# Optimization experiments

Measured on AMD Instinct MI355X. Metric: run time of the kernel, lower is better.

Reference implementation:

```python
import jax, jax.numpy as jnp
import numpy as np


def setup_inputs() -> dict:
    key = jax.random.key(0)
    kk, kq, kv = jax.random.split(key, 3)
    B, N, S, D = 2, 16, 2048, 64
    return {
        "k": jax.random.normal(kk, (B, N, S, D), dtype=jnp.float32),
        "q": jax.random.normal(kq, (B, N, S, D), dtype=jnp.float32),
        "v": jax.random.normal(kv, (B, N, S, D), dtype=jnp.float32),
    }


def reference(k, q, v):
    # NOTE: module applies no 1/sqrt(d) scaling (inputs pre-scaled upstream).
    attn_scores = jnp.einsum("bnqd,bnkd->bnqk", q, k)  # [B, N, Sq, Sk]
    attn_probs = jax.nn.softmax(attn_scores, axis=-1)
    # dropout p=0.0 -> identity
    attn_output = jnp.einsum("bnqk,bnkd->bnqd", attn_probs, v)
    return (attn_output, attn_probs)
```

## Files before the change

### kernel.cpp

```cpp
#include <hip/hip_runtime.h>

typedef _Float16 f16;
typedef _Float16 f16x8 __attribute__((ext_vector_type(8)));
typedef float f32x4 __attribute__((ext_vector_type(4)));

#define HEADS 32
#define SEQ   2048
#define DIM   64
#define QT    64
#define KT    64
#define NT    32
#define L2E   1.44269504088896340736f

__device__ __forceinline__ void gload_lds16(const void* gsrc, void* ldst) {
  __builtin_amdgcn_global_load_lds((__attribute__((address_space(1))) void*)gsrc,
                                   (__attribute__((address_space(3))) void*)ldst, 16, 0, 0);
}

__global__ __launch_bounds__(256) void prep_kernel(const float* __restrict__ k,
                                                   const float* __restrict__ v,
                                                   char* __restrict__ kt,
                                                   f16* __restrict__ vt) {
  int n = blockIdx.x * 256 + threadIdx.x;
  const int HALF = HEADS * SEQ * (DIM / 8);
  if (n < HALF) {
    int d8 = (n & 7) * 8;
    int kv = (n >> 3) & (SEQ - 1);
    int h  = n >> 14;
    const float* src = k + ((size_t)(h * SEQ + kv)) * DIM + d8;
    float4 a = *(const float4*)src;
    float4 b = *(const float4*)(src + 4);
    f16x8 o;
    o[0]=(f16)a.x; o[1]=(f16)a.y; o[2]=(f16)a.z; o[3]=(f16)a.w;
    o[4]=(f16)b.x; o[5]=(f16)b.y; o[6]=(f16)b.z; o[7]=(f16)b.w;
    *(f16x8*)(kt + ((size_t)(h * SEQ + kv)) * 128 + ((d8 * 2) ^ ((kv & 7) << 4))) = o;
  } else {
    int m = n - HALF;
    int d   = m & 63;
    int kv8 = ((m >> 6) & 255) * 8;
    int h   = m >> 14;
    const float* src = v + ((size_t)(h * SEQ + kv8)) * DIM + d;
    f16x8 o;
#pragma unroll
    for (int i = 0; i < 8; i++) o[i] = (f16)src[i * DIM];
    *(f16x8*)(vt + ((size_t)(h * DIM + d)) * SEQ + kv8) = o;
  }
}

#define STAGE(t, buf)                                                                  \
  do {                                                                                 \
    const char* ktile_ = kthead + (size_t)(t) * KT * 128;                              \
    gload_lds16(ktile_ + tid * 16, &lds_k[buf][tid * 16]);                             \
    gload_lds16(ktile_ + 4096 + tid * 16, &lds_k[buf][4096 + tid * 16]);               \
  } while (0)

#define QKT_M(SC, buf)                                                                 \
  do {                                                                                 \
    _Pragma("unroll") for (int kc = 0; kc < 2; kc++) {                                 \
      _Pragma("unroll") for (int f = 0; f < 4; f++) {                                  \
        int row_ = f * 16 + c;                                                         \
        f16x8 kb_ = *(const f16x8*)&lds_k[buf][row_ * 128 +                            \
                       ((kc * 64 + g * 16) ^ ((row_ & 7) << 4))];                      \
        SC[f] = __builtin_amdgcn_mfma_f32_16x16x32_f16(qa[kc], kb_, SC[f], 0, 0, 0);   \
      }                                                                                \
    }                                                                                  \
  } while (0)

#define LOAD_QA                                                                        \
  do {                                                                                 \
    const float* qp = q + ((size_t)(head * SEQ + q0 + w * 16 + c)) * DIM + g * 8;      \
    _Pragma("unroll") for (int kc = 0; kc < 2; kc++) {                                 \
      float4 a = *(const float4*)(qp + kc * 32);                                       \
      float4 b = *(const float4*)(qp + kc * 32 + 4);                                   \
      qa[kc][0]=(f16)a.x; qa[kc][1]=(f16)a.y; qa[kc][2]=(f16)a.z; qa[kc][3]=(f16)a.w;  \
      qa[kc][4]=(f16)b.x; qa[kc][5]=(f16)b.y; qa[kc][6]=(f16)b.z; qa[kc][7]=(f16)b.w;  \
    }                                                                                  \
  } while (0)

__global__ __launch_bounds__(256, 4) void lsum_kernel(const float* __restrict__ q,
                                                      const char* __restrict__ kt,
                                                      float* __restrict__ lsum) {
  __shared__ char lds_k[2][KT * 128];

  const int tid = threadIdx.x;
  const int w = tid >> 6, l = tid & 63, g = l >> 4, c = l & 15;
  const int swz  = (blockIdx.x & 7) * 128 + (blockIdx.x >> 3);
  const int head = swz >> 5;
  const int q0   = (swz & 31) * QT;

  f16x8 qa[2];
  LOAD_QA;
  const char* kthead = kt + (size_t)head * SEQ * 128;

  float l_ln[4] = {0.f, 0.f, 0.f, 0.f};
  STAGE(0, 0);
  __syncthreads();
  for (int t = 0; t < NT; t++) {
    int cur = t & 1;
    if (t + 1 < NT) STAGE(t + 1, cur ^ 1);
    f32x4 sc[4];
#pragma unroll
    for (int f = 0; f < 4; f++) sc[f] = (f32x4){0.f, 0.f, 0.f, 0.f};
    QKT_M(sc, cur);
#pragma unroll
    for (int f = 0; f < 4; f++)
#pragma unroll
      for (int r = 0; r < 4; r++) l_ln[r] += __builtin_amdgcn_exp2f(sc[f][r] * L2E);
    __syncthreads();
  }
#pragma unroll
  for (int r = 0; r < 4; r++) {
    float lv = l_ln[r];
#pragma unroll
    for (int d = 1; d < 16; d <<= 1) lv += __shfl_xor(lv, d, 64);
    if (c == 0) lsum[head * SEQ + q0 + w * 16 + 4 * g + r] = lv;
  }
}

__global__ __launch_bounds__(256, 4) void attn_kernel(const float* __restrict__ q,
                                                      const char* __restrict__ kt,
                                                      const f16* __restrict__ vt,
                                                      const float* __restrict__ lsum,
                                                      float* __restrict__ out_o,
                                                      float* __restrict__ out_p) {
  __shared__ char  lds_k[2][KT * 128];
  __shared__ float lds_pt[QT * 64];

  const int tid = threadIdx.x;
  const int w = tid >> 6, l = tid & 63, g = l >> 4, c = l & 15;
  const int swz  = (blockIdx.x & 7) * 128 + (blockIdx.x >> 3);
  const int head = swz >> 5;
  const int q0   = (swz & 31) * QT;

  f16x8 qa[2];
  LOAD_QA;

  const char* kthead = kt + (size_t)head * SEQ * 128;
  const f16*  vhead  = vt + (size_t)head * DIM * SEQ;

  f32x4 rinv;
#pragma unroll
  for (int r = 0; r < 4; r++)
    rinv[r] = 1.0f / lsum[head * SEQ + q0 + w * 16 + 4 * g + r];

  f32x4 o_acc[4];
#pragma unroll
  for (int f = 0; f < 4; f++) o_acc[f] = (f32x4){0.f, 0.f, 0.f, 0.f};
  float* prow = out_p + (size_t)(head * SEQ + q0) * SEQ;

  STAGE(0, 0);
  __syncthreads();
  for (int t = 0; t < NT; t++) {
    int cur = t & 1;
    if (t + 1 < NT) STAGE(t + 1, cur ^ 1);

    f16x8 vb[2][4];
#pragma unroll
    for (int kc = 0; kc < 2; kc++)
#pragma unroll
      for (int f = 0; f < 4; f++)
        vb[kc][f] = *(const f16x8*)(vhead + (size_t)(f * 16 + c) * SEQ + t * 64 + kc * 32 + g * 8);

    f32x4 sc[4];
#pragma unroll
    for (int f = 0; f < 4; f++) sc[f] = (f32x4){0.f, 0.f, 0.f, 0.f};
    QKT_M(sc, cur);

#pragma unroll
    for (int f = 0; f < 4; f++)
#pragma unroll
      for (int r = 0; r < 4; r++) {
        float pv = __builtin_amdgcn_exp2f(sc[f][r] * L2E) * rinv[r];
        int rowL = w * 16 + 4 * g + r;
        lds_pt[rowL * 64 + ((16 * f + c) ^ ((rowL & 7) << 2))] = pv;
      }
    asm volatile("" ::: "memory");

#pragma unroll
    for (int j = 0; j < 4; j++) {
      int rowL = w * 16 + j * 4 + g;
      f32x4 pv4 = *(const f32x4*)&lds_pt[rowL * 64 + ((c ^ (rowL & 7)) << 2)];
      __builtin_nontemporal_store(pv4, (f32x4*)&prow[(size_t)rowL * SEQ + t * 64 + c * 4]);
    }

    {
      int rowA = w * 16 + c;
      int sw = c & 7;
#pragma unroll
      for (int kc = 0; kc < 2; kc++) {
        f32x4 a0 = *(const f32x4*)&lds_pt[rowA * 64 + (((8 * kc + 2 * g) ^ sw) << 2)];
        f32x4 a1 = *(const f32x4*)&lds_pt[rowA * 64 + (((8 * kc + 2 * g + 1) ^ sw) << 2)];
        f16x8 pa;
        pa[0]=(f16)a0[0]; pa[1]=(f16)a0[1]; pa[2]=(f16)a0[2]; pa[3]=(f16)a0[3];
        pa[4]=(f16)a1[0]; pa[5]=(f16)a1[1]; pa[6]=(f16)a1[2]; pa[7]=(f16)a1[3];
#pragma unroll
        for (int f = 0; f < 4; f++)
          o_acc[f] = __builtin_amdgcn_mfma_f32_16x16x32_f16(pa, vb[kc][f], o_acc[f], 0, 0, 0);
      }
    }
    __syncthreads();
  }

#pragma unroll
  for (int f = 0; f < 4; f++)
#pragma unroll
    for (int r = 0; r < 4; r++) {
      int rowL = w * 16 + 4 * g + r;
      lds_pt[rowL * 64 + ((16 * f + c) ^ ((rowL & 7) << 2))] = o_acc[f][r];
    }
  asm volatile("" ::: "memory");
#pragma unroll
  for (int j = 0; j < 4; j++) {
    int rowL = w * 16 + j * 4 + g;
    f32x4 ov = *(const f32x4*)&lds_pt[rowL * 64 + ((c ^ (rowL & 7)) << 2)];
    __builtin_nontemporal_store(ov, (f32x4*)&out_o[(size_t)(head * SEQ + q0 + rowL) * DIM + c * 4]);
  }
}

extern "C" void kernel_launch(void* const* d_in, const int* in_sizes, int n_in,
                              void* d_out, int out_size, void* d_ws, size_t ws_size,
                              hipStream_t stream) {
  const float* k = (const float*)d_in[0];
  const float* q = (const float*)d_in[1];
  const float* v = (const float*)d_in[2];
  float* out_o = (float*)d_out;
  float* out_p = out_o + (size_t)HEADS * SEQ * DIM;

  char*  kt = (char*)d_ws;
  f16*   vt = (f16*)(kt + (size_t)HEADS * SEQ * DIM * 2);
  float* ls = (float*)(vt + (size_t)HEADS * SEQ * DIM);

  prep_kernel<<<dim3(4096), dim3(256), 0, stream>>>(k, v, kt, vt);
  lsum_kernel<<<dim3(1024), dim3(256), 0, stream>>>(q, kt, ls);
  attn_kernel<<<dim3(1024), dim3(256), 0, stream>>>(q, kt, vt, ls, out_o, out_p);
}
```

Measured before the change: 189.2 us.

## Store probabilities directly and stage fp16 P in LDS for PV MFMA

Removes the fp32 LDS transpose staging and writes the probability matrix and output straight from MFMA accumulator layout with scalar nontemporal stores. P is kept in LDS as fp16 with a swizzle so the PV MFMA operands load as single 16-byte vectors. The reciprocal of the row sum moves into the lsum kernel, and occupancy hints are raised. The cost is more, narrower global store instructions, which may hurt the dominant P write bandwidth.

```diff
diff --git a/kernel.cpp b/kernel.cpp
--- a/kernel.cpp
+++ b/kernel.cpp
@@ -77,9 +77,9 @@
     }                                                                                  \
   } while (0)
 
-__global__ __launch_bounds__(256, 4) void lsum_kernel(const float* __restrict__ q,
+__global__ __launch_bounds__(256, 8) void lsum_kernel(const float* __restrict__ q,
                                                       const char* __restrict__ kt,
-                                                      float* __restrict__ lsum) {
+                                                      float* __restrict__ rinv_out) {
   __shared__ char lds_k[2][KT * 128];
 
   const int tid = threadIdx.x;
@@ -113,18 +113,18 @@
     float lv = l_ln[r];
 #pragma unroll
     for (int d = 1; d < 16; d <<= 1) lv += __shfl_xor(lv, d, 64);
-    if (c == 0) lsum[head * SEQ + q0 + w * 16 + 4 * g + r] = lv;
-  }
-}
-
-__global__ __launch_bounds__(256, 4) void attn_kernel(const float* __restrict__ q,
+    if (c == 0) rinv_out[head * SEQ + q0 + w * 16 + 4 * g + r] = 1.0f / lv;
+  }
+}
+
+__global__ __launch_bounds__(256, 5) void attn_kernel(const float* __restrict__ q,
                                                       const char* __restrict__ kt,
                                                       const f16* __restrict__ vt,
-                                                      const float* __restrict__ lsum,
+                                                      const float* __restrict__ rinv_in,
                                                       float* __restrict__ out_o,
                                                       float* __restrict__ out_p) {
-  __shared__ char  lds_k[2][KT * 128];
-  __shared__ float lds_pt[QT * 64];
+  __shared__ char lds_k[2][KT * 128];
+  __shared__ char lds_p[QT * 128];
 
   const int tid = threadIdx.x;
   const int w = tid >> 6, l = tid & 63, g = l >> 4, c = l & 15;
@@ -141,7 +141,7 @@
   f32x4 rinv;
 #pragma unroll
   for (int r = 0; r < 4; r++)
-    rinv[r] = 1.0f / lsum[head * SEQ + q0 + w * 16 + 4 * g + r];
+    rinv[r] = rinv_in[head * SEQ + q0 + w * 16 + 4 * g + r];
 
   f32x4 o_acc[4];
 #pragma unroll
@@ -172,27 +172,17 @@
       for (int r = 0; r < 4; r++) {
         float pv = __builtin_amdgcn_exp2f(sc[f][r] * L2E) * rinv[r];
         int rowL = w * 16 + 4 * g + r;
-        lds_pt[rowL * 64 + ((16 * f + c) ^ ((rowL & 7) << 2))] = pv;
+        __builtin_nontemporal_store(pv, &prow[(size_t)rowL * SEQ + t * 64 + f * 16 + c]);
+        *(f16*)(lds_p + rowL * 128 + (((f * 16 + c) * 2) ^ ((rowL & 7) << 4))) = (f16)pv;
       }
     asm volatile("" ::: "memory");
 
-#pragma unroll
-    for (int j = 0; j < 4; j++) {
-      int rowL = w * 16 + j * 4 + g;
-      f32x4 pv4 = *(const f32x4*)&lds_pt[rowL * 64 + ((c ^ (rowL & 7)) << 2)];
-      __builtin_nontemporal_store(pv4, (f32x4*)&prow[(size_t)rowL * SEQ + t * 64 + c * 4]);
-    }
-
     {
       int rowA = w * 16 + c;
-      int sw = c & 7;
 #pragma unroll
       for (int kc = 0; kc < 2; kc++) {
-        f32x4 a0 = *(const f32x4*)&lds_pt[rowA * 64 + (((8 * kc + 2 * g) ^ sw) << 2)];
-        f32x4 a1 = *(const f32x4*)&lds_pt[rowA * 64 + (((8 * kc + 2 * g + 1) ^ sw) << 2)];
-        f16x8 pa;
-        pa[0]=(f16)a0[0]; pa[1]=(f16)a0[1]; pa[2]=(f16)a0[2]; pa[3]=(f16)a0[3];
-        pa[4]=(f16)a1[0]; pa[5]=(f16)a1[1]; pa[6]=(f16)a1[2]; pa[7]=(f16)a1[3];
+        f16x8 pa = *(const f16x8*)(lds_p + rowA * 128 +
+                                   ((kc * 64 + g * 16) ^ ((rowA & 7) << 4)));
 #pragma unroll
         for (int f = 0; f < 4; f++)
           o_acc[f] = __builtin_amdgcn_mfma_f32_16x16x32_f16(pa, vb[kc][f], o_acc[f], 0, 0, 0);
@@ -204,17 +194,9 @@
 #pragma unroll
   for (int f = 0; f < 4; f++)
 #pragma unroll
-    for (int r = 0; r < 4; r++) {
-      int rowL = w * 16 + 4 * g + r;
-      lds_pt[rowL * 64 + ((16 * f + c) ^ ((rowL & 7) << 2))] = o_acc[f][r];
-    }
-  asm volatile("" ::: "memory");
-#pragma unroll
-  for (int j = 0; j < 4; j++) {
-    int rowL = w * 16 + j * 4 + g;
-    f32x4 ov = *(const f32x4*)&lds_pt[rowL * 64 + ((c ^ (rowL & 7)) << 2)];
-    __builtin_nontemporal_store(ov, (f32x4*)&out_o[(size_t)(head * SEQ + q0 + rowL) * DIM + c * 4]);
-  }
+    for (int r = 0; r < 4; r++)
+      __builtin_nontemporal_store(o_acc[f][r],
+        &out_o[(size_t)(head * SEQ + q0 + w * 16 + 4 * g + r) * DIM + f * 16 + c]);
 }
 
 extern "C" void kernel_launch(void* const* d_in, const int* in_sizes, int n_in,
@@ -228,9 +210,9 @@
 
   char*  kt = (char*)d_ws;
   f16*   vt = (f16*)(kt + (size_t)HEADS * SEQ * DIM * 2);
-  float* ls = (float*)(vt + (size_t)HEADS * SEQ * DIM);
+  float* rs = (float*)(vt + (size_t)HEADS * SEQ * DIM);
 
   prep_kernel<<<dim3(4096), dim3(256), 0, stream>>>(k, v, kt, vt);
-  lsum_kernel<<<dim3(1024), dim3(256), 0, stream>>>(q, kt, ls);
-  attn_kernel<<<dim3(1024), dim3(256), 0, stream>>>(q, kt, vt, ls, out_o, out_p);
-}
+  lsum_kernel<<<dim3(1024), dim3(256), 0, stream>>>(q, kt, rs);
+  attn_kernel<<<dim3(1024), dim3(256), 0, stream>>>(q, kt, vt, rs, out_o, out_p);
+}
```

New measurement: 232.4 us. 22.8% more time.

## Triple-buffer K in lsum kernel and replace syncthreads with explicit vmcnt waits

Applied to the files above, without the earlier changes.

The row-sum kernel moves to a three-stage LDS ring for K tiles, prefetches two tiles ahead, and raises its occupancy hint to 8 blocks per CU. Full __syncthreads barriers become raw s_barrier calls with explicit vmcnt waits and sched_barrier fences, so outstanding async loads are not drained every iteration. In the attention kernel the next-K staging is issued after the V register loads, and a partial vmcnt wait is placed before the PV MFMAs. The reciprocal of the row sum is now computed once in the lsum kernel rather than in each attention block. The hand-counted vmcnt values are fragile: if the compiler's load/store counts differ from what was assumed, data may be read before it arrives.

```diff
diff --git a/kernel.cpp b/kernel.cpp
--- a/kernel.cpp
+++ b/kernel.cpp
@@ -77,10 +77,16 @@
     }                                                                                  \
   } while (0)
 
-__global__ __launch_bounds__(256, 4) void lsum_kernel(const float* __restrict__ q,
+#define VMCNT(N) asm volatile("s_waitcnt vmcnt(" #N ")" ::: "memory");                 \
+                 __builtin_amdgcn_sched_barrier(0)
+#define BAR()    __builtin_amdgcn_sched_barrier(0);                                    \
+                 __builtin_amdgcn_s_barrier();                                         \
+                 __builtin_amdgcn_sched_barrier(0)
+
+__global__ __launch_bounds__(256, 8) void lsum_kernel(const float* __restrict__ q,
                                                       const char* __restrict__ kt,
-                                                      float* __restrict__ lsum) {
-  __shared__ char lds_k[2][KT * 128];
+                                                      float* __restrict__ rinv_out) {
+  __shared__ char lds_k[3][KT * 128];
 
   const int tid = threadIdx.x;
   const int w = tid >> 6, l = tid & 63, g = l >> 4, c = l & 15;
@@ -94,33 +100,34 @@
 
   float l_ln[4] = {0.f, 0.f, 0.f, 0.f};
   STAGE(0, 0);
+  STAGE(1, 1);
   __syncthreads();
   for (int t = 0; t < NT; t++) {
-    int cur = t & 1;
-    if (t + 1 < NT) STAGE(t + 1, cur ^ 1);
+    if (t + 2 < NT) STAGE(t + 2, (t + 2) % 3);
     f32x4 sc[4];
 #pragma unroll
     for (int f = 0; f < 4; f++) sc[f] = (f32x4){0.f, 0.f, 0.f, 0.f};
-    QKT_M(sc, cur);
+    QKT_M(sc, t % 3);
 #pragma unroll
     for (int f = 0; f < 4; f++)
 #pragma unroll
       for (int r = 0; r < 4; r++) l_ln[r] += __builtin_amdgcn_exp2f(sc[f][r] * L2E);
-    __syncthreads();
+    VMCNT(2);
+    BAR();
   }
 #pragma unroll
   for (int r = 0; r < 4; r++) {
     float lv = l_ln[r];
 #pragma unroll
     for (int d = 1; d < 16; d <<= 1) lv += __shfl_xor(lv, d, 64);
-    if (c == 0) lsum[head * SEQ + q0 + w * 16 + 4 * g + r] = lv;
+    if (c == 0) rinv_out[head * SEQ + q0 + w * 16 + 4 * g + r] = 1.0f / lv;
   }
 }
 
 __global__ __launch_bounds__(256, 4) void attn_kernel(const float* __restrict__ q,
                                                       const char* __restrict__ kt,
                                                       const f16* __restrict__ vt,
-                                                      const float* __restrict__ lsum,
+                                                      const float* __restrict__ rinv_in,
                                                       float* __restrict__ out_o,
                                                       float* __restrict__ out_p) {
   __shared__ char  lds_k[2][KT * 128];
@@ -141,7 +148,7 @@
   f32x4 rinv;
 #pragma unroll
   for (int r = 0; r < 4; r++)
-    rinv[r] = 1.0f / lsum[head * SEQ + q0 + w * 16 + 4 * g + r];
+    rinv[r] = rinv_in[head * SEQ + q0 + w * 16 + 4 * g + r];
 
   f32x4 o_acc[4];
 #pragma unroll
@@ -152,7 +159,6 @@
   __syncthreads();
   for (int t = 0; t < NT; t++) {
     int cur = t & 1;
-    if (t + 1 < NT) STAGE(t + 1, cur ^ 1);
 
     f16x8 vb[2][4];
 #pragma unroll
@@ -160,6 +166,8 @@
 #pragma unroll
       for (int f = 0; f < 4; f++)
         vb[kc][f] = *(const f16x8*)(vhead + (size_t)(f * 16 + c) * SEQ + t * 64 + kc * 32 + g * 8);
+
+    if (t + 1 < NT) STAGE(t + 1, cur ^ 1);
 
     f32x4 sc[4];
 #pragma unroll
@@ -183,6 +191,8 @@
       __builtin_nontemporal_store(pv4, (f32x4*)&prow[(size_t)rowL * SEQ + t * 64 + c * 4]);
     }
 
+    VMCNT(6);
+
     {
       int rowA = w * 16 + c;
       int sw = c & 7;
@@ -198,7 +208,8 @@
           o_acc[f] = __builtin_amdgcn_mfma_f32_16x16x32_f16(pa, vb[kc][f], o_acc[f], 0, 0, 0);
       }
     }
-    __syncthreads();
+
+    BAR();
   }
 
 #pragma unroll
@@ -228,9 +239,9 @@
 
   char*  kt = (char*)d_ws;
   f16*   vt = (f16*)(kt + (size_t)HEADS * SEQ * DIM * 2);
-  float* ls = (float*)(vt + (size_t)HEADS * SEQ * DIM);
+  float* rs = (float*)(vt + (size_t)HEADS * SEQ * DIM);
 
   prep_kernel<<<dim3(4096), dim3(256), 0, stream>>>(k, v, kt, vt);
-  lsum_kernel<<<dim3(1024), dim3(256), 0, stream>>>(q, kt, ls);
-  attn_kernel<<<dim3(1024), dim3(256), 0, stream>>>(q, kt, vt, ls, out_o, out_p);
-}
+  lsum_kernel<<<dim3(1024), dim3(256), 0, stream>>>(q, kt, rs);
+  attn_kernel<<<dim3(1024), dim3(256), 0, stream>>>(q, kt, vt, rs, out_o, out_p);
+}
```

After: 195.6 us. +3.3%, slower.
